# Optimization experiments

Hardware: AMD Instinct MI355X
Metric: run time of the kernel (lower is better)

## Reference

```python
import jax, jax.numpy as jnp
import numpy as np

GAMMA = 2.2
EPS = 1e-08


def _up2(x):
    B, C, H, W = x.shape
    return jax.image.resize(x, (B, C, 2 * H, 2 * W), method='bilinear')


def _pixel_unshuffle2(x):
    # [B,1,2H,2W] -> [B,4,H,W], torch channel order (ry, rx)
    B, C, H2, W2 = x.shape
    H, W = H2 // 2, W2 // 2
    x = x.reshape(B, C, H, 2, W, 2)
    x = x.transpose(0, 1, 3, 5, 2, 4)
    return x.reshape(B, C * 4, H, W)


def _pixel_shuffle2(x):
    # [B,4,H,W] -> [B,1,2H,2W]
    B, C4, H, W = x.shape
    C = C4 // 4
    x = x.reshape(B, C, 2, 2, H, W)
    x = x.transpose(0, 1, 4, 2, 5, 3)
    return x.reshape(B, C, 2 * H, 2 * W)


def _demosaic(bayer):
    # bayer: [B,4,H,W] packed RGGB planes -> [B,3,2H,2W]
    red = _up2(bayer[:, 0:1])

    gr = jnp.flip(bayer[:, 1:2], axis=-1)
    gr = jnp.flip(_up2(gr), axis=-1)
    gr = _pixel_unshuffle2(gr)  # [B,4,H,W]

    gb = jnp.flip(bayer[:, 2:3], axis=-2)
    gb = jnp.flip(_up2(gb), axis=-2)
    gb = _pixel_unshuffle2(gb)  # [B,4,H,W]

    green = jnp.stack([
        (gr[:, 0] + gb[:, 0]) * 0.5,  # green at red site
        gr[:, 1],                      # green at green-red site
        gb[:, 2],                      # green at green-blue site
        (gr[:, 3] + gb[:, 3]) * 0.5,  # green at blue site
    ], axis=1)
    green = _pixel_shuffle2(green)  # [B,1,2H,2W]

    blue = jnp.flip(bayer[:, 3:4], axis=-1)
    blue = jnp.flip(_up2(blue), axis=-1)

    return jnp.concatenate([red, green, blue], axis=1)


def _isp(x, awb_gains, ccms):
    if x.shape[1] == 4:
        x = _demosaic(x)
    x = x * 2.0
    x = x[:, ::-1]  # channel order [2,1,0]
    x = jnp.einsum('bchw,bck->bkhw', x, awb_gains)  # awb_en=1, clip=0
    x = jnp.einsum('bchw,bck->bkhw', x, ccms)       # ccm_en=1, clip=0
    x = x[:, ::-1]
    # gamma compression
    return jnp.clip(x, EPS) ** jnp.float32(1.0 / GAMMA)


def setup_inputs() -> dict:
    key = jax.random.key(0)
    k1, k2, k3, k4, k5 = jax.random.split(key, 5)
    B, H, W = 8, 512, 512
    return {
        'pred': jax.random.uniform(k1, (B, 4, H, W), dtype=jnp.float32),
        'gt': jax.random.uniform(k2, (B, 4, H, W), dtype=jnp.float32),
        'awb': jax.random.uniform(k3, (B, 3, 3), dtype=jnp.float32),
        'cam2rgb': jax.random.uniform(k4, (B, 3, 3), dtype=jnp.float32),
        'rgb_gain': jax.random.uniform(k5, (B,), dtype=jnp.float32),
    }


def reference(pred, gt, awb, cam2rgb, rgb_gain):
    # rgb_gain (dgain) is accepted but unused, matching the torch module.
    x = _isp(pred, awb, cam2rgb)
    y = _isp(gt, awb, cam2rgb)
    return (x, y)
```

## Files before the change

### kernel.cpp

```cpp
#include <hip/hip_runtime.h>


#define GAMMA_INV 0.45454545454545453f
#define EPS_CLIP 1e-8f

__device__ __forceinline__ float4 up2_quad(const float* __restrict__ p,
                                           int jm, int j, int jp,
                                           int im, int i, int ip) {
  const int W = 512;
  const float* r0 = p + jm * W;
  const float* r1 = p + j  * W;
  const float* r2 = p + jp * W;
  float a0 = r0[im], a1 = r0[i], a2 = r0[ip];
  float b0 = r1[im], b1 = r1[i], b2 = r1[ip];
  float c0 = r2[im], c1 = r2[i], c2 = r2[ip];
  float e0 = 0.25f * a0 + 0.75f * b0;
  float e1 = 0.25f * a1 + 0.75f * b1;
  float e2 = 0.25f * a2 + 0.75f * b2;
  float o0 = 0.75f * b0 + 0.25f * c0;
  float o1 = 0.75f * b1 + 0.25f * c1;
  float o2 = 0.75f * b2 + 0.25f * c2;
  float4 r;
  r.x = 0.25f * e0 + 0.75f * e1;
  r.y = 0.75f * e1 + 0.25f * e2;
  r.z = 0.25f * o0 + 0.75f * o1;
  r.w = 0.75f * o1 + 0.25f * o2;
  return r;
}

__device__ __forceinline__ float gamma_enc(float v) {
  v = fmaxf(v, EPS_CLIP);
  return exp2f(GAMMA_INV * log2f(v));
}

__global__ __launch_bounds__(256) void isp_kernel(
    const float* __restrict__ pred, const float* __restrict__ gt,
    const float* __restrict__ awb, const float* __restrict__ ccm,
    float* __restrict__ out) {
  constexpr int H = 512, W = 512;
  constexpr int HW = H * W;
  constexpr long long OUT_IMG = 8LL * 3 * 1024 * 1024;

  int idx = blockIdx.x * blockDim.x + threadIdx.x;
  int i = idx & (W - 1);
  int j = (idx >> 9) & (H - 1);
  int b = idx >> 18;

  const float* A  = awb + b * 9;
  const float* Cm = ccm + b * 9;
  float M[3][3];
#pragma unroll
  for (int k = 0; k < 3; ++k) {
#pragma unroll
    for (int e = 0; e < 3; ++e) {
      int ar = (2 - e) * 3;
      int cc = 2 - k;
      M[k][e] = 2.0f * (A[ar + 0] * Cm[0 + cc] +
                        A[ar + 1] * Cm[3 + cc] +
                        A[ar + 2] * Cm[6 + cc]);
    }
  }

  int jm = (j > 0) ? j - 1 : 0;
  int jp = (j < H - 1) ? j + 1 : H - 1;
  int im = (i > 0) ? i - 1 : 0;
  int ip = (i < W - 1) ? i + 1 : W - 1;

  int oy = 2 * j, ox = 2 * i;

#pragma unroll
  for (int img = 0; img < 2; ++img) {
    const float* src = (img == 0 ? pred : gt) + (long long)b * 4 * HW;
    float* dst = out + (long long)img * OUT_IMG;

    float4 R  = up2_quad(src + 0 * HW, jm, j, jp, im, i, ip);
    float4 Gr = up2_quad(src + 1 * HW, jm, j, jp, im, i, ip);
    float4 Gb = up2_quad(src + 2 * HW, jm, j, jp, im, i, ip);
    float4 Bl = up2_quad(src + 3 * HW, jm, j, jp, im, i, ip);

    float r[4]  = {R.x, R.y, R.z, R.w};
    float g[4]  = {0.5f * (Gr.x + Gb.x), Gr.y, Gb.z, 0.5f * (Gr.w + Gb.w)};
    float bl[4] = {Bl.x, Bl.y, Bl.z, Bl.w};

    float o[3][4];
#pragma unroll
    for (int px = 0; px < 4; ++px) {
#pragma unroll
      for (int k = 0; k < 3; ++k) {
        float v = M[k][0] * r[px] + M[k][1] * g[px] + M[k][2] * bl[px];
        o[k][px] = gamma_enc(v);
      }
    }

#pragma unroll
    for (int k = 0; k < 3; ++k) {
      long long obase = ((long long)(b * 3 + k) * 1024 + oy) * 1024 + ox;
      float2 top = make_float2(o[k][0], o[k][1]);
      float2 bot = make_float2(o[k][2], o[k][3]);
      *reinterpret_cast<float2*>(dst + obase) = top;
      *reinterpret_cast<float2*>(dst + obase + 1024) = bot;
    }
  }
}

extern "C" void kernel_launch(void* const* d_in, const int* in_sizes, int n_in,
                              void* d_out, int out_size, void* d_ws, size_t ws_size,
                              hipStream_t stream) {
  const float* pred = (const float*)d_in[0];
  const float* gt   = (const float*)d_in[1];
  const float* awb  = (const float*)d_in[2];
  const float* ccm  = (const float*)d_in[3];
  float* out = (float*)d_out;

  const int total = 8 * 512 * 512;
  dim3 block(256);
  dim3 grid(total / 256);
  isp_kernel<<<grid, block, 0, stream>>>(pred, gt, awb, ccm, out);
}
```

Baseline: 273.5 us.

## Coarsen ISP threads to four input columns with vectorized loads and stores

```diff
diff --git a/kernel.cpp b/kernel.cpp
--- a/kernel.cpp
+++ b/kernel.cpp
@@ -4,33 +4,42 @@
 #define GAMMA_INV 0.45454545454545453f
 #define EPS_CLIP 1e-8f
 
-__device__ __forceinline__ float4 up2_quad(const float* __restrict__ p,
-                                           int jm, int j, int jp,
-                                           int im, int i, int ip) {
-  const int W = 512;
-  const float* r0 = p + jm * W;
-  const float* r1 = p + j  * W;
-  const float* r2 = p + jp * W;
-  float a0 = r0[im], a1 = r0[i], a2 = r0[ip];
-  float b0 = r1[im], b1 = r1[i], b2 = r1[ip];
-  float c0 = r2[im], c1 = r2[i], c2 = r2[ip];
-  float e0 = 0.25f * a0 + 0.75f * b0;
-  float e1 = 0.25f * a1 + 0.75f * b1;
-  float e2 = 0.25f * a2 + 0.75f * b2;
-  float o0 = 0.75f * b0 + 0.25f * c0;
-  float o1 = 0.75f * b1 + 0.25f * c1;
-  float o2 = 0.75f * b2 + 0.25f * c2;
-  float4 r;
-  r.x = 0.25f * e0 + 0.75f * e1;
-  r.y = 0.75f * e1 + 0.25f * e2;
-  r.z = 0.25f * o0 + 0.75f * o1;
-  r.w = 0.75f * o1 + 0.25f * o2;
-  return r;
+__device__ __forceinline__ float gamma_enc(float v) {
+  v = fmaxf(v, EPS_CLIP);
+  return exp2f(GAMMA_INV * __log2f(v));
 }
 
-__device__ __forceinline__ float gamma_enc(float v) {
-  v = fmaxf(v, EPS_CLIP);
-  return exp2f(GAMMA_INV * log2f(v));
+__device__ __forceinline__ void load_row(const float* __restrict__ row,
+                                         int im, int i, int ip, float w[6]) {
+  float4 v = *reinterpret_cast<const float4*>(row + i);
+  w[0] = row[im];
+  w[1] = v.x; w[2] = v.y; w[3] = v.z; w[4] = v.w;
+  w[5] = row[ip];
+}
+
+__device__ __forceinline__ void up2_row4(const float* __restrict__ ch,
+                                         int jm, int j, int jp,
+                                         int im, int i, int ip,
+                                         float top[8], float bot[8]) {
+  const int W = 512;
+  float w0[6], w1[6], w2[6];
+  load_row(ch + jm * W, im, i, ip, w0);
+  load_row(ch + j  * W, im, i, ip, w1);
+  load_row(ch + jp * W, im, i, ip, w2);
+  float e[6], o[6];
+#pragma unroll
+  for (int c = 0; c < 6; ++c) {
+    e[c] = 0.25f * w0[c] + 0.75f * w1[c];
+    o[c] = 0.75f * w1[c] + 0.25f * w2[c];
+  }
+#pragma unroll
+  for (int p = 0; p < 4; ++p) {
+    int wp = p + 1;
+    top[2 * p]     = 0.25f * e[wp - 1] + 0.75f * e[wp];
+    top[2 * p + 1] = 0.75f * e[wp]     + 0.25f * e[wp + 1];
+    bot[2 * p]     = 0.25f * o[wp - 1] + 0.75f * o[wp];
+    bot[2 * p + 1] = 0.75f * o[wp]     + 0.25f * o[wp + 1];
+  }
 }
 
 __global__ __launch_bounds__(256) void isp_kernel(
@@ -42,9 +51,10 @@
   constexpr long long OUT_IMG = 8LL * 3 * 1024 * 1024;
 
   int idx = blockIdx.x * blockDim.x + threadIdx.x;
-  int i = idx & (W - 1);
-  int j = (idx >> 9) & (H - 1);
-  int b = idx >> 18;
+  int t   = idx & 127;
+  int j   = (idx >> 7) & 511;
+  int b   = (idx >> 16) & 7;
+  int img = idx >> 19;
 
   const float* A  = awb + b * 9;
   const float* Cm = ccm + b * 9;
@@ -61,45 +71,44 @@
     }
   }
 
+  int i  = 4 * t;
   int jm = (j > 0) ? j - 1 : 0;
   int jp = (j < H - 1) ? j + 1 : H - 1;
   int im = (i > 0) ? i - 1 : 0;
-  int ip = (i < W - 1) ? i + 1 : W - 1;
+  int ip = (i + 4 < W) ? i + 4 : W - 1;
 
-  int oy = 2 * j, ox = 2 * i;
+  const float* src = (img ? gt : pred) + (long long)b * 4 * HW;
+
+  float rT[8], rB[8], gT[8], gB[8], bT[8], bB[8];
+  float tT[8], tB[8];
+
+  up2_row4(src + 0 * HW, jm, j, jp, im, i, ip, rT, rB);
+  up2_row4(src + 1 * HW, jm, j, jp, im, i, ip, gT, gB);
+  up2_row4(src + 2 * HW, jm, j, jp, im, i, ip, tT, tB);
+#pragma unroll
+  for (int p = 0; p < 4; ++p) {
+    gT[2 * p]     = 0.5f * (gT[2 * p] + tT[2 * p]);
+    gB[2 * p]     = tB[2 * p];
+    gB[2 * p + 1] = 0.5f * (gB[2 * p + 1] + tB[2 * p + 1]);
+  }
+  up2_row4(src + 3 * HW, jm, j, jp, im, i, ip, bT, bB);
+
+  int oy = 2 * j, ox = 8 * t;
+  float* dst = out + (long long)img * OUT_IMG;
 
 #pragma unroll
-  for (int img = 0; img < 2; ++img) {
-    const float* src = (img == 0 ? pred : gt) + (long long)b * 4 * HW;
-    float* dst = out + (long long)img * OUT_IMG;
-
-    float4 R  = up2_quad(src + 0 * HW, jm, j, jp, im, i, ip);
-    float4 Gr = up2_quad(src + 1 * HW, jm, j, jp, im, i, ip);
-    float4 Gb = up2_quad(src + 2 * HW, jm, j, jp, im, i, ip);
-    float4 Bl = up2_quad(src + 3 * HW, jm, j, jp, im, i, ip);
-
-    float r[4]  = {R.x, R.y, R.z, R.w};
-    float g[4]  = {0.5f * (Gr.x + Gb.x), Gr.y, Gb.z, 0.5f * (Gr.w + Gb.w)};
-    float bl[4] = {Bl.x, Bl.y, Bl.z, Bl.w};
-
-    float o[3][4];
+  for (int k = 0; k < 3; ++k) {
+    float oT[8], oB[8];
 #pragma unroll
-    for (int px = 0; px < 4; ++px) {
-#pragma unroll
-      for (int k = 0; k < 3; ++k) {
-        float v = M[k][0] * r[px] + M[k][1] * g[px] + M[k][2] * bl[px];
-        o[k][px] = gamma_enc(v);
-      }
+    for (int p = 0; p < 8; ++p) {
+      oT[p] = gamma_enc(M[k][0] * rT[p] + M[k][1] * gT[p] + M[k][2] * bT[p]);
+      oB[p] = gamma_enc(M[k][0] * rB[p] + M[k][1] * gB[p] + M[k][2] * bB[p]);
     }
-
-#pragma unroll
-    for (int k = 0; k < 3; ++k) {
-      long long obase = ((long long)(b * 3 + k) * 1024 + oy) * 1024 + ox;
-      float2 top = make_float2(o[k][0], o[k][1]);
-      float2 bot = make_float2(o[k][2], o[k][3]);
-      *reinterpret_cast<float2*>(dst + obase) = top;
-      *reinterpret_cast<float2*>(dst + obase + 1024) = bot;
-    }
+    long long obase = ((long long)(b * 3 + k) * 1024 + oy) * 1024 + ox;
+    *reinterpret_cast<float4*>(dst + obase)          = make_float4(oT[0], oT[1], oT[2], oT[3]);
+    *reinterpret_cast<float4*>(dst + obase + 4)      = make_float4(oT[4], oT[5], oT[6], oT[7]);
+    *reinterpret_cast<float4*>(dst + obase + 1024)     = make_float4(oB[0], oB[1], oB[2], oB[3]);
+    *reinterpret_cast<float4*>(dst + obase + 1028)     = make_float4(oB[4], oB[5], oB[6], oB[7]);
   }
 }
 
@@ -112,7 +121,7 @@
   const float* ccm  = (const float*)d_in[3];
   float* out = (float*)d_out;
 
-  const int total = 8 * 512 * 512;
+  const int total = 2 * 8 * 512 * 128;
   dim3 block(256);
   dim3 grid(total / 256);
   isp_kernel<<<grid, block, 0, stream>>>(pred, gt, awb, ccm, out);
```

New measurement: 271.5 us. Within noise of the previous version (-0.7%).
